# Optimization experiments

Measured on AMD Instinct MI355X. Metric: run time of the kernel, lower is better.

The kernel has to match this reference:

```python
import jax, jax.numpy as jnp
import numpy as np

SEQ, IN, H = 65536, 64, 128


def setup_inputs() -> dict:
    key = jax.random.key(0)
    ks = jax.random.split(key, 7)
    s_i, s_h = 1.0 / np.sqrt(IN), 1.0 / np.sqrt(H)
    return {
        "input_seq": jax.random.normal(ks[0], (SEQ, IN), jnp.float32),
        "W_ih": jax.random.normal(ks[1], (4 * H, IN), jnp.float32) * s_i,
        "W_hh": jax.random.normal(ks[2], (4 * H, H), jnp.float32) * s_h,
        "b_ih": jax.random.normal(ks[3], (4 * H,), jnp.float32) * s_h,
        "b_hh": jax.random.normal(ks[4], (4 * H,), jnp.float32) * s_h,
        "W_lin": jax.random.normal(ks[5], (1, H), jnp.float32) * s_h,
        "b_lin": jax.random.normal(ks[6], (1,), jnp.float32) * s_h,
    }


def reference(input_seq, W_ih, W_hh, b_ih, b_hh, W_lin, b_lin):
    # Precompute input contributions to all gates: [SEQ, 4H]
    x_gates = input_seq @ W_ih.T + b_ih + b_hh

    def step(carry, xg):
        h, c = carry
        gates = xg + h @ W_hh.T  # [4H]
        i, f, g, o = jnp.split(gates, 4)
        i = jax.nn.sigmoid(i)
        f = jax.nn.sigmoid(f)
        g = jnp.tanh(g)
        o = jax.nn.sigmoid(o)
        c = f * c + i * g
        h = o * jnp.tanh(c)
        return (h, c), None

    h0 = jnp.zeros((H,), input_seq.dtype)
    c0 = jnp.zeros((H,), input_seq.dtype)
    (hT, _), _ = jax.lax.scan(step, (h0, c0), x_gates)
    # outputs[-1] == sigmoid(linear(h_T)); shape [1]
    return jax.nn.sigmoid(hT @ W_lin.T + b_lin)
```

## Files before the change

kernel.cpp:

```cpp
#include <hip/hip_runtime.h>

#define SEQ 65536
#define IN_DIM 64
#define H 128
#define G4 512

typedef _Float16 half_t;
typedef half_t half2_t __attribute__((ext_vector_type(2)));
typedef half_t half8_t __attribute__((ext_vector_type(8)));

__device__ __forceinline__ float fast_rcp(float x) { return __builtin_amdgcn_rcpf(x); }

__device__ __forceinline__ float sigmoid_f(float x) {
    x = fminf(fmaxf(x, -30.f), 30.f);
    return fast_rcp(1.f + __expf(-x));
}

#if __has_builtin(__builtin_amdgcn_fdot2)
__device__ __forceinline__ float dot2(half2_t a, half2_t b, float c) {
    return __builtin_amdgcn_fdot2(a, b, c, false);
}
#else
__device__ __forceinline__ float dot2(half2_t a, half2_t b, float c) {
    return c + (float)a[0] * (float)b[0] + (float)a[1] * (float)b[1];
}
#endif

__device__ __forceinline__ half2_t pick2(half8_t v, int i0) {
    half2_t r; r[0] = v[i0]; r[1] = v[i0 + 1]; return r;
}

__device__ __forceinline__ half8_t cvt8(const float* p) {
    float4 a = *(const float4*)p;
    float4 b = *(const float4*)(p + 4);
    half8_t r;
    r[0] = (half_t)a.x; r[1] = (half_t)a.y; r[2] = (half_t)a.z; r[3] = (half_t)a.w;
    r[4] = (half_t)b.x; r[5] = (half_t)b.y; r[6] = (half_t)b.z; r[7] = (half_t)b.w;
    return r;
}

template <int CTRL>
__device__ __forceinline__ float qperm(float x) {
    return __int_as_float(
        __builtin_amdgcn_mov_dpp(__float_as_int(x), CTRL, 0xF, 0xF, true));
}
#define qx1(x)  qperm<0xB1>(x)
#define qx2(x)  qperm<0x4E>(x)
#define qrev(x) qperm<0x1B>(x)

__global__ __launch_bounds__(256) void xg_gemm(
    const float* __restrict__ x, const float* __restrict__ Wih,
    const float* __restrict__ bih, const float* __restrict__ bhh,
    float* __restrict__ xg)
{
    long long gid = (long long)blockIdx.x * 256 + threadIdx.x;
    int s = (int)(gid >> 9);
    int r = (int)(gid & 511);
    const float* xr = x + (long long)s * IN_DIM;
    const float* wr = Wih + (long long)r * IN_DIM;
    float a0 = 0.f, a1 = 0.f, a2 = 0.f, a3 = 0.f;
#pragma unroll
    for (int k = 0; k < IN_DIM; k += 4) {
        float4 iv = *(const float4*)(xr + k);
        float4 wv = *(const float4*)(wr + k);
        a0 += wv.x * iv.x; a1 += wv.y * iv.y;
        a2 += wv.z * iv.z; a3 += wv.w * iv.w;
    }
    xg[gid] = (a0 + a1) + (a2 + a3) + bih[r] + bhh[r];
}

__global__ __launch_bounds__(256, 1) void lstm_scan(
    const float* __restrict__ Whh, const float* __restrict__ Wlin,
    const float* __restrict__ blin, const float* __restrict__ xg,
    float* __restrict__ out)
{
    __shared__ __align__(16) half_t shbuf[2][H];
    const int tid = threadIdx.x;
    const int ql = tid & 3;
    const int j0 = (tid >> 2) * 2;
    const int c0 = ql * 32;

#define LOADW(P, ROW)                                                     \
    half8_t P##0 = cvt8(Whh + (size_t)(ROW) * H + c0 + 0),                \
            P##1 = cvt8(Whh + (size_t)(ROW) * H + c0 + 8),                \
            P##2 = cvt8(Whh + (size_t)(ROW) * H + c0 + 16),               \
            P##3 = cvt8(Whh + (size_t)(ROW) * H + c0 + 24);
    LOADW(wi0, j0)           LOADW(wi1, j0 + 1)
    LOADW(wf0, 128 + j0)     LOADW(wf1, 129 + j0)
    LOADW(wg0, 256 + j0)     LOADW(wg1, 257 + j0)
    LOADW(wo0, 384 + j0)     LOADW(wo1, 385 + j0)
#undef LOADW
#define PIN(A, B, C, D) asm volatile("" : "+v"(A), "+v"(B), "+v"(C), "+v"(D))
    PIN(wi00, wi01, wi02, wi03); PIN(wi10, wi11, wi12, wi13);
    PIN(wf00, wf01, wf02, wf03); PIN(wf10, wf11, wf12, wf13);
    PIN(wg00, wg01, wg02, wg03); PIN(wg10, wg11, wg12, wg13);
    PIN(wo00, wo01, wo02, wo03); PIN(wo10, wo11, wo12, wo13);
#undef PIN

    const bool isg = (ql == 2);
    const bool l0  = (ql == 0);
    const float* xgbase = xg + ql * H + j0;
    float c = 0.f;

    float2 xg_c = *(const float2*)(xgbase + (size_t)0 * G4);
    float2 xg_n = *(const float2*)(xgbase + (size_t)1 * G4);

    if (tid < H) shbuf[0][tid] = (half_t)0.f;
    __syncthreads();

#define DOT8(ACC, WV, HV)                                                 \
    ACC = dot2(pick2(WV, 0), pick2(HV, 0), ACC);                          \
    ACC = dot2(pick2(WV, 2), pick2(HV, 2), ACC);                          \
    ACC = dot2(pick2(WV, 4), pick2(HV, 4), ACC);                          \
    ACC = dot2(pick2(WV, 6), pick2(HV, 6), ACC);
#define DOTROW(ACC, P)                                                    \
    DOT8(ACC, P##0, h0) DOT8(ACC, P##1, h1)                               \
    DOT8(ACC, P##2, h2) DOT8(ACC, P##3, h3)
#define QRED(X) X += qx1(X); X += qx2(X);

#define STEP(RB, WB, T)                                                   \
    {                                                                     \
        const half8_t* hp = (const half8_t*)&shbuf[RB][c0];               \
        half8_t h0 = hp[0], h1 = hp[1], h2 = hp[2], h3 = hp[3];           \
        int tp = (T) + 2; if (tp > SEQ - 1) tp = SEQ - 1;                 \
        float2 xg_p = *(const float2*)(xgbase + (size_t)tp * G4);         \
        float ai0 = 0.f, ai1 = 0.f, af0 = 0.f, af1 = 0.f;                 \
        float ag0 = 0.f, ag1 = 0.f, ao0 = 0.f, ao1 = 0.f;                 \
        DOTROW(ai0, wi0) DOTROW(ai1, wi1)                                 \
        DOTROW(af0, wf0) DOTROW(af1, wf1)                                 \
        DOTROW(ag0, wg0) DOTROW(ag1, wg1)                                 \
        DOTROW(ao0, wo0) DOTROW(ao1, wo1)                                 \
        QRED(ai0) QRED(ai1) QRED(af0) QRED(af1)                           \
        QRED(ag0) QRED(ag1) QRED(ao0) QRED(ao1)                           \
                         \
        float sa = ai0, sb = ai1;                                         \
        if (ql == 1) { sa = af0; sb = af1; }                              \
        if (ql == 2) { sa = ag0; sb = ag1; }                              \
        if (ql == 3) { sa = ao0; sb = ao1; }                              \
        float xa = sa + xg_c.x, xb = sb + xg_c.y;                         \
        float ua = isg ? xa + xa : xa;                                    \
        float ub = isg ? xb + xb : xb;                                    \
        float ra = sigmoid_f(ua), rb = sigmoid_f(ub);                     \
        float gva = isg ? ra + ra - 1.f : ra;        \
        float gvb = isg ? rb + rb - 1.f : rb;                             \
          \
        float fA = qx1(gva), iB = qx1(gvb);                               \
        float gA = qx2(gva), oB = qx2(gvb);                               \
        float oA = qrev(gva), gB = qrev(gvb);                             \
        float ii = l0 ? gva : iB;                                         \
        float ff = l0 ? fA  : gvb;                                        \
        float gg = l0 ? gA  : gB;                                         \
        float oo = l0 ? oA  : oB;                                         \
        c = ff * c + ii * gg;                                             \
        float th = 2.f * sigmoid_f(c + c) - 1.f;                          \
        float hh = oo * th;                                               \
        if (ql < 2) shbuf[WB][j0 + ql] = (half_t)hh;                      \
        asm volatile("s_waitcnt lgkmcnt(0)" ::: "memory");                \
        __builtin_amdgcn_s_barrier();                                     \
        __builtin_amdgcn_sched_barrier(0);                                \
        xg_c = xg_n; xg_n = xg_p;                                         \
    }

    for (int t = 0; t < SEQ; t += 2) {
        STEP(0, 1, t)
        STEP(1, 0, t + 1)
    }
#undef STEP
#undef QRED
#undef DOTROW
#undef DOT8

    if (tid < 64) {
        float p = (float)shbuf[0][tid] * Wlin[tid] +
                  (float)shbuf[0][tid + 64] * Wlin[tid + 64];
#pragma unroll
        for (int off = 32; off > 0; off >>= 1) p += __shfl_down(p, off);
        if (tid == 0) out[0] = sigmoid_f(p + blin[0]);
    }
}

__global__ __launch_bounds__(512, 2) void lstm_scan_fb(
    const float* __restrict__ x, const float* __restrict__ Wih,
    const float* __restrict__ Whh, const float* __restrict__ bih,
    const float* __restrict__ bhh, const float* __restrict__ Wlin,
    const float* __restrict__ blin, float* __restrict__ out)
{
    __shared__ __align__(16) half_t sh_h[H];
    __shared__ __align__(16) float  sh_g[G4];
    const int row = threadIdx.x;
    const float* wrow = Whh + (long long)row * H;

    half8_t w0  = cvt8(wrow + 0),   w1  = cvt8(wrow + 8);
    half8_t w2  = cvt8(wrow + 16),  w3  = cvt8(wrow + 24);
    half8_t w4  = cvt8(wrow + 32),  w5  = cvt8(wrow + 40);
    half8_t w6  = cvt8(wrow + 48),  w7  = cvt8(wrow + 56);
    half8_t w8  = cvt8(wrow + 64),  w9  = cvt8(wrow + 72);
    half8_t w10 = cvt8(wrow + 80),  w11 = cvt8(wrow + 88);
    half8_t w12 = cvt8(wrow + 96),  w13 = cvt8(wrow + 104);
    half8_t w14 = cvt8(wrow + 112), w15 = cvt8(wrow + 120);

    const float bsum = bih[row] + bhh[row];
    float c = 0.f;
    if (row < H) sh_h[row] = (half_t)0.f;

    float xg_cur;
    {
        float a = bsum;
        const float* wir = Wih + (long long)row * IN_DIM;
#pragma unroll
        for (int k = 0; k < IN_DIM; k += 4) {
            float4 iv = *(const float4*)(x + k);
            float4 wv = *(const float4*)(wir + k);
            a += wv.x * iv.x + wv.y * iv.y + wv.z * iv.z + wv.w * iv.w;
        }
        xg_cur = a;
    }
    const bool is_g = (row >= 2 * H) && (row < 3 * H);
    __syncthreads();

    const half8_t* hch = (const half8_t*)sh_h;

    for (int t = 0; t < SEQ; ++t) {
        float xg_nxt = 0.f;
        if (t + 1 < SEQ) {
            const float* xr = x + (size_t)(t + 1) * IN_DIM;
            const float* wir = Wih + (long long)row * IN_DIM;
            float a = bsum;
#pragma unroll
            for (int k = 0; k < IN_DIM; k += 4) {
                float4 iv = *(const float4*)(xr + k);
                float4 wv = *(const float4*)(wir + k);
                a += wv.x * iv.x + wv.y * iv.y + wv.z * iv.z + wv.w * iv.w;
            }
            xg_nxt = a;
        }
        float a0 = 0.f, a1 = 0.f, a2 = 0.f, a3 = 0.f;
#define DOTC(WV, CI)                                                     \
        {   half8_t hv = hch[CI];                                        \
            a0 = dot2(pick2(WV, 0), pick2(hv, 0), a0);                   \
            a1 = dot2(pick2(WV, 2), pick2(hv, 2), a1);                   \
            a2 = dot2(pick2(WV, 4), pick2(hv, 4), a2);                   \
            a3 = dot2(pick2(WV, 6), pick2(hv, 6), a3); }
        DOTC(w0, 0)  DOTC(w1, 1)  DOTC(w2, 2)   DOTC(w3, 3)
        DOTC(w4, 4)  DOTC(w5, 5)  DOTC(w6, 6)   DOTC(w7, 7)
        DOTC(w8, 8)  DOTC(w9, 9)  DOTC(w10, 10) DOTC(w11, 11)
        DOTC(w12, 12) DOTC(w13, 13) DOTC(w14, 14) DOTC(w15, 15)
#undef DOTC
        float pre = xg_cur + ((a0 + a1) + (a2 + a3));
        float gv;
        if (is_g) {
            float s = sigmoid_f(pre + pre);
            gv = s + s - 1.f;
        } else {
            gv = sigmoid_f(pre);
        }
        sh_g[row] = gv;
        __syncthreads();
        if (row >= 3 * H) {
            int j = row - 3 * H;
            float ig = sh_g[j];
            float fg = sh_g[H + j];
            float gg = sh_g[2 * H + j];
            c = fg * c + ig * gg;
            float s = sigmoid_f(c + c);
            sh_h[j] = (half_t)(gv * (s + s - 1.f));
        }
        __syncthreads();
        xg_cur = xg_nxt;
    }

    if (row < 64) {
        float p = (float)sh_h[row] * Wlin[row] +
                  (float)sh_h[row + 64] * Wlin[row + 64];
#pragma unroll
        for (int off = 32; off > 0; off >>= 1) p += __shfl_down(p, off);
        if (row == 0) out[0] = sigmoid_f(p + blin[0]);
    }
}

extern "C" void kernel_launch(void* const* d_in, const int* in_sizes, int n_in,
                              void* d_out, int out_size, void* d_ws, size_t ws_size,
                              hipStream_t stream)
{
    const float* x    = (const float*)d_in[0];
    const float* Wih  = (const float*)d_in[1];
    const float* Whh  = (const float*)d_in[2];
    const float* bih  = (const float*)d_in[3];
    const float* bhh  = (const float*)d_in[4];
    const float* Wlin = (const float*)d_in[5];
    const float* blin = (const float*)d_in[6];
    float* out = (float*)d_out;

    const size_t need = (size_t)SEQ * G4 * sizeof(float);
    if (ws_size >= need) {
        float* xg = (float*)d_ws;
        xg_gemm<<<(SEQ * G4) / 256, 256, 0, stream>>>(x, Wih, bih, bhh, xg);
        lstm_scan<<<1, 256, 0, stream>>>(Whh, Wlin, blin, xg, out);
    } else {
        lstm_scan_fb<<<1, 512, 0, stream>>>(x, Wih, Whh, bih, bhh, Wlin,
                                            blin, out);
    }
}
```

Baseline: 32.30 ms.

## Split LSTM recurrence over 512 threads, one hidden unit per quad

The scan kernel moves from 256 threads, each holding two hidden units' weight rows, to 512 threads where each quad of lanes owns one hidden unit and computes all four gates redundantly. This drops the cross-lane gate exchange. The xg GEMM output is interleaved so each quad reads its i/f/g/o inputs with one float4 load, and the sigmoid input clamp is removed. The serial critical path shrinks to fewer dot products per lane, at the cost of more waves syncing at each barrier, redundant transcendental work, and possible overflow behaviour without the clamp.

```diff
diff --git a/kernel.cpp b/kernel.cpp
--- a/kernel.cpp
+++ b/kernel.cpp
@@ -12,7 +12,6 @@
 __device__ __forceinline__ float fast_rcp(float x) { return __builtin_amdgcn_rcpf(x); }
 
 __device__ __forceinline__ float sigmoid_f(float x) {
-    x = fminf(fmaxf(x, -30.f), 30.f);
     return fast_rcp(1.f + __expf(-x));
 }
 
@@ -46,7 +45,6 @@
 }
 #define qx1(x)  qperm<0xB1>(x)
 #define qx2(x)  qperm<0x4E>(x)
-#define qrev(x) qperm<0x1B>(x)
 
 __global__ __launch_bounds__(256) void xg_gemm(
     const float* __restrict__ x, const float* __restrict__ Wih,
@@ -55,9 +53,11 @@
 {
     long long gid = (long long)blockIdx.x * 256 + threadIdx.x;
     int s = (int)(gid >> 9);
-    int r = (int)(gid & 511);
+    int rr = (int)(gid & 511);
+    int j = rr >> 2, g = rr & 3;
+    int row = g * H + j;
     const float* xr = x + (long long)s * IN_DIM;
-    const float* wr = Wih + (long long)r * IN_DIM;
+    const float* wr = Wih + (long long)row * IN_DIM;
     float a0 = 0.f, a1 = 0.f, a2 = 0.f, a3 = 0.f;
 #pragma unroll
     for (int k = 0; k < IN_DIM; k += 4) {
@@ -66,10 +66,10 @@
         a0 += wv.x * iv.x; a1 += wv.y * iv.y;
         a2 += wv.z * iv.z; a3 += wv.w * iv.w;
     }
-    xg[gid] = (a0 + a1) + (a2 + a3) + bih[r] + bhh[r];
-}
-
-__global__ __launch_bounds__(256, 1) void lstm_scan(
+    xg[gid] = (a0 + a1) + (a2 + a3) + bih[row] + bhh[row];
+}
+
+__global__ __launch_bounds__(512, 2) void lstm_scan(
     const float* __restrict__ Whh, const float* __restrict__ Wlin,
     const float* __restrict__ blin, const float* __restrict__ xg,
     float* __restrict__ out)
@@ -77,7 +77,7 @@
     __shared__ __align__(16) half_t shbuf[2][H];
     const int tid = threadIdx.x;
     const int ql = tid & 3;
-    const int j0 = (tid >> 2) * 2;
+    const int j  = tid >> 2;
     const int c0 = ql * 32;
 
 #define LOADW(P, ROW)                                                     \
@@ -85,25 +85,17 @@
             P##1 = cvt8(Whh + (size_t)(ROW) * H + c0 + 8),                \
             P##2 = cvt8(Whh + (size_t)(ROW) * H + c0 + 16),               \
             P##3 = cvt8(Whh + (size_t)(ROW) * H + c0 + 24);
-    LOADW(wi0, j0)           LOADW(wi1, j0 + 1)
-    LOADW(wf0, 128 + j0)     LOADW(wf1, 129 + j0)
-    LOADW(wg0, 256 + j0)     LOADW(wg1, 257 + j0)
-    LOADW(wo0, 384 + j0)     LOADW(wo1, 385 + j0)
+    LOADW(wi, j)
+    LOADW(wf, 128 + j)
+    LOADW(wg, 256 + j)
+    LOADW(wo, 384 + j)
 #undef LOADW
-#define PIN(A, B, C, D) asm volatile("" : "+v"(A), "+v"(B), "+v"(C), "+v"(D))
-    PIN(wi00, wi01, wi02, wi03); PIN(wi10, wi11, wi12, wi13);
-    PIN(wf00, wf01, wf02, wf03); PIN(wf10, wf11, wf12, wf13);
-    PIN(wg00, wg01, wg02, wg03); PIN(wg10, wg11, wg12, wg13);
-    PIN(wo00, wo01, wo02, wo03); PIN(wo10, wo11, wo12, wo13);
-#undef PIN
-
-    const bool isg = (ql == 2);
-    const bool l0  = (ql == 0);
-    const float* xgbase = xg + ql * H + j0;
+
+    const float* xgq = xg + (size_t)j * 4;
     float c = 0.f;
 
-    float2 xg_c = *(const float2*)(xgbase + (size_t)0 * G4);
-    float2 xg_n = *(const float2*)(xgbase + (size_t)1 * G4);
+    float4 xg_c = *(const float4*)(xgq + (size_t)0 * G4);
+    float4 xg_n = *(const float4*)(xgq + (size_t)1 * G4);
 
     if (tid < H) shbuf[0][tid] = (half_t)0.f;
     __syncthreads();
@@ -113,9 +105,6 @@
     ACC = dot2(pick2(WV, 2), pick2(HV, 2), ACC);                          \
     ACC = dot2(pick2(WV, 4), pick2(HV, 4), ACC);                          \
     ACC = dot2(pick2(WV, 6), pick2(HV, 6), ACC);
-#define DOTROW(ACC, P)                                                    \
-    DOT8(ACC, P##0, h0) DOT8(ACC, P##1, h1)                               \
-    DOT8(ACC, P##2, h2) DOT8(ACC, P##3, h3)
 #define QRED(X) X += qx1(X); X += qx2(X);
 
 #define STEP(RB, WB, T)                                                   \
@@ -123,38 +112,31 @@
         const half8_t* hp = (const half8_t*)&shbuf[RB][c0];               \
         half8_t h0 = hp[0], h1 = hp[1], h2 = hp[2], h3 = hp[3];           \
         int tp = (T) + 2; if (tp > SEQ - 1) tp = SEQ - 1;                 \
-        float2 xg_p = *(const float2*)(xgbase + (size_t)tp * G4);         \
+        float4 xg_p = *(const float4*)(xgq + (size_t)tp * G4);            \
         float ai0 = 0.f, ai1 = 0.f, af0 = 0.f, af1 = 0.f;                 \
         float ag0 = 0.f, ag1 = 0.f, ao0 = 0.f, ao1 = 0.f;                 \
-        DOTROW(ai0, wi0) DOTROW(ai1, wi1)                                 \
-        DOTROW(af0, wf0) DOTROW(af1, wf1)                                 \
-        DOTROW(ag0, wg0) DOTROW(ag1, wg1)                                 \
-        DOTROW(ao0, wo0) DOTROW(ao1, wo1)                                 \
-        QRED(ai0) QRED(ai1) QRED(af0) QRED(af1)                           \
-        QRED(ag0) QRED(ag1) QRED(ao0) QRED(ao1)                           \
-                         \
-        float sa = ai0, sb = ai1;                                         \
-        if (ql == 1) { sa = af0; sb = af1; }                              \
-        if (ql == 2) { sa = ag0; sb = ag1; }                              \
-        if (ql == 3) { sa = ao0; sb = ao1; }                              \
-        float xa = sa + xg_c.x, xb = sb + xg_c.y;                         \
-        float ua = isg ? xa + xa : xa;                                    \
-        float ub = isg ? xb + xb : xb;                                    \
-        float ra = sigmoid_f(ua), rb = sigmoid_f(ub);                     \
-        float gva = isg ? ra + ra - 1.f : ra;        \
-        float gvb = isg ? rb + rb - 1.f : rb;                             \
-          \
-        float fA = qx1(gva), iB = qx1(gvb);                               \
-        float gA = qx2(gva), oB = qx2(gvb);                               \
-        float oA = qrev(gva), gB = qrev(gvb);                             \
-        float ii = l0 ? gva : iB;                                         \
-        float ff = l0 ? fA  : gvb;                                        \
-        float gg = l0 ? gA  : gB;                                         \
-        float oo = l0 ? oA  : oB;                                         \
-        c = ff * c + ii * gg;                                             \
-        float th = 2.f * sigmoid_f(c + c) - 1.f;                          \
-        float hh = oo * th;                                               \
-        if (ql < 2) shbuf[WB][j0 + ql] = (half_t)hh;                      \
+        DOT8(ai0, wi0, h0) DOT8(ai1, wi1, h1)                             \
+        DOT8(ai0, wi2, h2) DOT8(ai1, wi3, h3)                             \
+        DOT8(af0, wf0, h0) DOT8(af1, wf1, h1)                             \
+        DOT8(af0, wf2, h2) DOT8(af1, wf3, h3)                             \
+        DOT8(ag0, wg0, h0) DOT8(ag1, wg1, h1)                             \
+        DOT8(ag0, wg2, h2) DOT8(ag1, wg3, h3)                             \
+        DOT8(ao0, wo0, h0) DOT8(ao1, wo1, h1)                             \
+        DOT8(ao0, wo2, h2) DOT8(ao1, wo3, h3)                             \
+        float si = ai0 + ai1, sf = af0 + af1;                             \
+        float sg = ag0 + ag1, so = ao0 + ao1;                             \
+        QRED(si) QRED(sf) QRED(sg) QRED(so)                               \
+        float gi = sigmoid_f(si + xg_c.x);                                \
+        float gf = sigmoid_f(sf + xg_c.y);                                \
+        float ug = sg + xg_c.z;                                           \
+        float s2 = sigmoid_f(ug + ug);                                    \
+        float gg = s2 + s2 - 1.f;                 \
+        float go = sigmoid_f(so + xg_c.w);                                \
+        c = gf * c + gi * gg;                                             \
+        float sc = sigmoid_f(c + c);                                      \
+        float th = sc + sc - 1.f;                                         \
+        float hh = go * th;                                               \
+        if (ql == 0) shbuf[WB][j] = (half_t)hh;                           \
         asm volatile("s_waitcnt lgkmcnt(0)" ::: "memory");                \
         __builtin_amdgcn_s_barrier();                                     \
         __builtin_amdgcn_sched_barrier(0);                                \
@@ -167,7 +149,6 @@
     }
 #undef STEP
 #undef QRED
-#undef DOTROW
 #undef DOT8
 
     if (tid < 64) {
@@ -257,13 +238,13 @@
         sh_g[row] = gv;
         __syncthreads();
         if (row >= 3 * H) {
-            int j = row - 3 * H;
-            float ig = sh_g[j];
-            float fg = sh_g[H + j];
-            float gg = sh_g[2 * H + j];
+            int jj = row - 3 * H;
+            float ig = sh_g[jj];
+            float fg = sh_g[H + jj];
+            float gg = sh_g[2 * H + jj];
             c = fg * c + ig * gg;
             float s = sigmoid_f(c + c);
-            sh_h[j] = (half_t)(gv * (s + s - 1.f));
+            sh_h[jj] = (half_t)(gv * (s + s - 1.f));
         }
         __syncthreads();
         xg_cur = xg_nxt;
@@ -295,7 +276,7 @@
     if (ws_size >= need) {
         float* xg = (float*)d_ws;
         xg_gemm<<<(SEQ * G4) / 256, 256, 0, stream>>>(x, Wih, bih, bhh, xg);
-        lstm_scan<<<1, 256, 0, stream>>>(Whh, Wlin, blin, xg, out);
+        lstm_scan<<<1, 512, 0, stream>>>(Whh, Wlin, blin, xg, out);
     } else {
         lstm_scan_fb<<<1, 512, 0, stream>>>(x, Wih, Whh, bih, bhh, Wlin,
                                             blin, out);
```

New measurement: 37.05 ms. 1.15x slower.
